# Performance work log

Hardware: AMD Instinct MI355X
Metric: run time of the kernel (lower is better)

The kernel has to match this reference:

```python
import jax, jax.numpy as jnp
import numpy as np

E = 8      # num_experts
K = 2      # num_experts_per_tok
D = 1024   # n_embd
H = 1024   # expert_dim (= 2*n_embd // k)
B, T = 2, 1024


def setup_inputs() -> dict:
    key = jax.random.key(0)
    ks = jax.random.split(key, 6)
    s = 0.02  # weight init scale (keeps relu^2 activations tame)
    return {
        "x": jax.random.normal(ks[0], (B, T, D), dtype=jnp.float32),
        "gate_w": jax.random.normal(ks[1], (E, D), dtype=jnp.float32) * s,
        "lb_bias": jnp.zeros((E,), dtype=jnp.float32),
        "w1": jax.random.normal(ks[2], (E, H, D), dtype=jnp.float32) * s,
        "w2": jax.random.normal(ks[3], (E, D, H), dtype=jnp.float32) * s,
        "cfc": jax.random.normal(ks[4], (H, D), dtype=jnp.float32) * s,
        "cproj": jax.random.normal(ks[5], (D, H), dtype=jnp.float32) * s,
    }


def reference(x, gate_w, lb_bias, w1, w2, cfc, cproj):
    Bx, Tx, Dx = x.shape
    # --- Router: top-k over (logits + load-balance bias), sigmoid gating ---
    logits = jnp.einsum('btd,ed->bte', x, gate_w)               # (B,T,E)
    _, idx = jax.lax.top_k(logits + lb_bias, K)                  # (B,T,K)
    sel_logits = jnp.take_along_axis(logits, idx, axis=-1)       # (B,T,K)
    w = jax.nn.sigmoid(sel_logits)
    w = w / (jnp.sum(w, axis=-1, keepdims=True) + 1e-6)          # (B,T,K)

    # --- Dispatch/combine (dense-equivalent of the per-expert gather loop) ---
    xf = x.reshape(-1, Dx)                                       # (N,D)
    idxf = idx.reshape(-1, K)                                    # (N,K)
    wf = w.reshape(-1, K)                                        # (N,K)
    onehot = jax.nn.one_hot(idxf, E, dtype=wf.dtype)             # (N,K,E)
    we = jnp.einsum('nke,nk->ne', onehot, wf)                    # combined per-expert weight (N,E)

    hidden = jnp.square(jax.nn.relu(jnp.einsum('nd,ehd->neh', xf, w1)))  # (N,E,H)
    expert_out = jnp.einsum('neh,edh->ned', hidden, w2)                  # (N,E,D)
    moe_out = jnp.einsum('ned,ne->nd', expert_out, we).reshape(Bx, Tx, Dx)

    # --- Shared expert (always active): relu(x W1^T)^2 W2^T ---
    sh = jnp.square(jax.nn.relu(jnp.einsum('btd,hd->bth', x, cfc)))
    shared = jnp.einsum('bth,dh->btd', sh, cproj)
    return moe_out + shared
```

## Files before the change

kernel.cpp:

```cpp
#include <hip/hip_runtime.h>
#include <stdint.h>

#define D_DIM 1024
#define H_DIM 1024
#define NE 8
#define NTOK 2048
#define SB 5120
#define TOTAL_ROWS 7168
#define GEMM_BLKS 224
#define CONV2_BLKS 2304
#define M8 (8 * 1024 * 1024)

typedef __bf16 bf16;
typedef bf16 bf16x8 __attribute__((ext_vector_type(8)));
typedef float f32x4 __attribute__((ext_vector_type(4)));

#define GL16(SRC, DST)                                               \
  __builtin_amdgcn_global_load_lds(                                  \
      (const __attribute__((address_space(1))) void*)(SRC),          \
      (__attribute__((address_space(3))) void*)(DST), 16, 0, 0)

#define WS_NTILES     0
#define WS_TILE_E     64
#define WS_TILE_BASE  576
#define WS_EIDX       2048
#define WS_WTOK       18432
#define WS_TOK        34816
#define WS_SLOT       63488
#define WS_XG         131072
#define WS_HID        16777216
#define WS_W1B        33554432
#define WS_W2B        50331648
#define WS_CFCB       67108864
#define WS_CPROJB     69206016

__global__ __launch_bounds__(256) void convrouter(
    const float* __restrict__ x, const float* __restrict__ gw,
    const float* __restrict__ lb, int* __restrict__ eidx,
    float* __restrict__ wtok, bf16* __restrict__ xg,
    const float* __restrict__ w1, const float* __restrict__ cfc,
    bf16* __restrict__ w1b, bf16* __restrict__ cfcb) {
  const int bx = blockIdx.x;
  if (bx >= 512) {
    int i = ((bx - 512) * 256 + threadIdx.x) * 8;
    const float* s;
    bf16* d;
    if (i < M8) { s = w1 + i;        d = w1b + i; }
    else        { s = cfc + (i - M8); d = cfcb + (i - M8); }
    float4 a = *(const float4*)(s);
    float4 b = *(const float4*)(s + 4);
    union { uint4 v; bf16 h[8]; } t;
    t.h[0] = (bf16)a.x; t.h[1] = (bf16)a.y; t.h[2] = (bf16)a.z; t.h[3] = (bf16)a.w;
    t.h[4] = (bf16)b.x; t.h[5] = (bf16)b.y; t.h[6] = (bf16)b.z; t.h[7] = (bf16)b.w;
    *(uint4*)(d) = t.v;
    return;
  }
  const int wave = threadIdx.x >> 6;
  const int lane = threadIdx.x & 63;
  const int n = bx * 4 + wave;

  const float4* xr = (const float4*)(x + (size_t)n * D_DIM);
  float4 xv[4];
#pragma unroll
  for (int q = 0; q < 4; q++) xv[q] = xr[q * 64 + lane];

  float acc[NE];
#pragma unroll
  for (int e = 0; e < NE; e++) acc[e] = 0.f;
#pragma unroll
  for (int e = 0; e < NE; e++) {
    const float4* gr = (const float4*)(gw + e * D_DIM);
#pragma unroll
    for (int q = 0; q < 4; q++) {
      float4 g = gr[q * 64 + lane];
      acc[e] += xv[q].x * g.x + xv[q].y * g.y + xv[q].z * g.z + xv[q].w * g.w;
    }
  }

  bf16* dst = xg + (size_t)n * D_DIM;
#pragma unroll
  for (int q = 0; q < 4; q++) {
    union { ushort4 u; bf16 h[4]; } t;
    t.h[0] = (bf16)xv[q].x; t.h[1] = (bf16)xv[q].y;
    t.h[2] = (bf16)xv[q].z; t.h[3] = (bf16)xv[q].w;
    *(ushort4*)(dst + (q * 64 + lane) * 4) = t.u;
  }

#pragma unroll
  for (int e = 0; e < NE; e++)
#pragma unroll
    for (int off = 32; off > 0; off >>= 1) acc[e] += __shfl_xor(acc[e], off, 64);

  if (lane == 0) {
    float b[NE];
#pragma unroll
    for (int e = 0; e < NE; e++) b[e] = acc[e] + lb[e];
    int i0 = 0; float v0 = b[0];
#pragma unroll
    for (int e = 1; e < NE; e++) if (b[e] > v0) { v0 = b[e]; i0 = e; }
    int i1 = -1; float v1 = -3.4e38f;
#pragma unroll
    for (int e = 0; e < NE; e++) if (e != i0 && b[e] > v1) { v1 = b[e]; i1 = e; }
    float s0 = 1.f / (1.f + expf(-acc[i0]));
    float s1 = 1.f / (1.f + expf(-acc[i1]));
    float s = s0 + s1 + 1e-6f;
    eidx[n * 2] = i0;     wtok[n * 2] = s0 / s;
    eidx[n * 2 + 1] = i1; wtok[n * 2 + 1] = s1 / s;
  }
}

__global__ __launch_bounds__(256) void assign_kernel(
    const int* __restrict__ eidx, int* __restrict__ tE, int* __restrict__ tB,
    int* __restrict__ ntiles, int* __restrict__ tok,
    int* __restrict__ slotIdx) {
  __shared__ int segCnt[64][NE];
  __shared__ int segBase[64][NE];
  const int tid = threadIdx.x;
  const int wave = tid >> 6, lane = tid & 63;
  const unsigned long long below = (lane == 0) ? 0ull : ((~0ull) >> (64 - lane));

  int e16[16], pr16[16];
#pragma unroll
  for (int t = 0; t < 16; t++) {
    const int r = t * 256 + tid;
    const int seg = t * 4 + wave;
    const int e = eidx[r];
    int prior = 0;
#pragma unroll
    for (int ee = 0; ee < NE; ee++) {
      unsigned long long m = __ballot(e == ee);
      if (e == ee) prior = __popcll(m & below);
      if (lane == ee) segCnt[seg][ee] = __popcll(m);
    }
    e16[t] = e; pr16[t] = prior;
  }

  for (int s = tid; s < TOTAL_ROWS; s += 256) {
    tok[s] = (s < SB) ? 0 : (s - SB);
  }
  __syncthreads();

  if (wave == 0) {
    int v[NE], inc[NE];
#pragma unroll
    for (int e = 0; e < NE; e++) { v[e] = segCnt[lane][e]; inc[e] = v[e]; }
#pragma unroll
    for (int off = 1; off < 64; off <<= 1) {
#pragma unroll
      for (int e = 0; e < NE; e++) {
        int u = __shfl_up(inc[e], off);
        if (lane >= off) inc[e] += u;
      }
    }
    int tot[NE];
#pragma unroll
    for (int e = 0; e < NE; e++) tot[e] = __shfl(inc[e], 63);
    int offsL[NE]; int b = 0;
#pragma unroll
    for (int e = 0; e < NE; e++) { offsL[e] = b; b += ((tot[e] + 127) >> 7) << 7; }
#pragma unroll
    for (int e = 0; e < NE; e++) segBase[lane][e] = offsL[e] + (inc[e] - v[e]);
    if (lane == 0) {
      int nt = 0;
      for (int e = 0; e < NE; e++) {
        int t128 = (tot[e] + 127) >> 7;
        for (int t = 0; t < t128; t++) { tE[nt] = e; tB[nt] = offsL[e] + t * 128; nt++; }
      }
      for (int t = 0; t < 16; t++) { tE[nt] = NE; tB[nt] = SB + t * 128; nt++; }
      ntiles[0] = nt;
      ntiles[1] = (nt * 4 + 7) >> 3;
    }
  }
  __syncthreads();

#pragma unroll
  for (int t = 0; t < 16; t++) {
    const int r = t * 256 + tid;
    const int seg = t * 4 + wave;
    const int slot = segBase[seg][e16[t]] + pr16[t];
    tok[slot] = r >> 1;
    slotIdx[r] = slot;
  }
}

template <int MODE>
__global__ __launch_bounds__(512) void moe_gemm(
    const bf16* __restrict__ Ab, const bf16* __restrict__ We,
    const bf16* __restrict__ Ws, const int* __restrict__ tE,
    const int* __restrict__ tB, const int* __restrict__ ntp,
    bf16* __restrict__ Cout, const int* __restrict__ tok,
    const float* __restrict__ cvs1, const float* __restrict__ cvs2,
    bf16* __restrict__ cvd1, bf16* __restrict__ cvd2) {
  if (MODE == 0 && blockIdx.x >= GEMM_BLKS) {
    int i = ((blockIdx.x - GEMM_BLKS) * 512 + threadIdx.x) * 8;
    const float* s;
    bf16* d;
    if (i < M8) { s = cvs1 + i;        d = cvd1 + i; }
    else        { s = cvs2 + (i - M8); d = cvd2 + (i - M8); }
    float4 a = *(const float4*)(s);
    float4 b = *(const float4*)(s + 4);
    union { uint4 v; bf16 h[8]; } t;
    t.h[0] = (bf16)a.x; t.h[1] = (bf16)a.y; t.h[2] = (bf16)a.z; t.h[3] = (bf16)a.w;
    t.h[4] = (bf16)b.x; t.h[5] = (bf16)b.y; t.h[6] = (bf16)b.z; t.h[7] = (bf16)b.w;
    *(uint4*)(d) = t.v;
    return;
  }

  const int per = ntp[1];
  const int g = blockIdx.x & 7, idx = blockIdx.x >> 3;
  if (idx >= per) return;
  const int p = g * per + idx;
  if (p >= ntp[0] * 4) return;
  const int mslot = p >> 2;
  const int n0 = (p & 3) * 256;
  const int e = tE[mslot];
  const int base = tB[mslot];
  const bf16* Bp = (e < NE) ? (We + (size_t)e * (H_DIM * D_DIM)) : Ws;

  __shared__ bf16 As[3 * 4096];
  __shared__ bf16 Bs[3 * 8192];

  const int tid = threadIdx.x;
  const int wave = tid >> 6, lane = tid & 63;

  const int rS = tid >> 2, sS = tid & 3;
  const int cS = sS ^ ((rS >> 1) & 3);
  size_t rowA;
  if (MODE == 0) rowA = tok[base + rS];
  else           rowA = base + rS;
  const bf16* gA  = Ab + rowA * 1024 + cS * 8;
  const bf16* gB1 = Bp + (size_t)(n0 + rS) * 1024 + cS * 8;
  const bf16* gB2 = Bp + (size_t)(n0 + 128 + rS) * 1024 + cS * 8;
  bf16* laBase = As + tid * 8;
  bf16* lbBase = Bs + tid * 8;

  const int wm = (wave >> 2) * 64, wn = (wave & 3) * 64;
  const int fr = lane & 15, chk = lane >> 4;
  int aOff[4], bOff[4];
#pragma unroll
  for (int i = 0; i < 4; i++) {
    const int r = wm + i * 16 + fr;
    aOff[i] = r * 32 + ((chk ^ ((r >> 1) & 3)) * 8);
  }
#pragma unroll
  for (int j = 0; j < 4; j++) {
    const int r = wn + j * 16 + fr;
    bOff[j] = r * 32 + ((chk ^ ((r >> 1) & 3)) * 8);
  }

  const f32x4 zero = {0.f, 0.f, 0.f, 0.f};
  f32x4 acc[4][4];
#pragma unroll
  for (int i = 0; i < 4; i++)
#pragma unroll
    for (int j = 0; j < 4; j++) acc[i][j] = zero;

#pragma unroll
  for (int t = 0; t < 3; ++t) {
    const int ko = t * 32;
    GL16(gA + ko,  laBase + t * 4096);
    GL16(gB1 + ko, lbBase + t * 8192);
    GL16(gB2 + ko, lbBase + t * 8192 + 4096);
  }

#define GEMM_ITER(KT, VMSTR, ISSUE)                                           \
  {                                                                           \
    const int cur = (KT) % 3;                                                 \
    asm volatile("s_waitcnt vmcnt(" VMSTR ")" ::: "memory");                  \
    __builtin_amdgcn_s_barrier();              \
    __builtin_amdgcn_sched_barrier(0);                                        \
    bf16x8 af[4], bv[4];                                                      \
    _Pragma("unroll") for (int i = 0; i < 4; i++)                             \
        af[i] = *(const bf16x8*)&As[cur * 4096 + aOff[i]];                    \
    _Pragma("unroll") for (int j = 0; j < 4; j++)                             \
        bv[j] = *(const bf16x8*)&Bs[cur * 8192 + bOff[j]];                    \
    asm volatile("s_waitcnt lgkmcnt(0)" ::: "memory");                        \
    __builtin_amdgcn_s_barrier();             \
    __builtin_amdgcn_sched_barrier(0);                                        \
    if (ISSUE) {                                                              \
      const int ko = ((KT) + 3) * 32;                                         \
      GL16(gA + ko,  laBase + cur * 4096);                                    \
      GL16(gB1 + ko, lbBase + cur * 8192);                                    \
      GL16(gB2 + ko, lbBase + cur * 8192 + 4096);                             \
    }                                                                         \
    __builtin_amdgcn_s_setprio(1);                                            \
    _Pragma("unroll") for (int i = 0; i < 4; i++)                             \
      _Pragma("unroll") for (int j = 0; j < 4; j++)                           \
          acc[i][j] = __builtin_amdgcn_mfma_f32_16x16x32_bf16(                \
              af[i], bv[j], acc[i][j], 0, 0, 0);                              \
    __builtin_amdgcn_s_setprio(0);                                            \
  }

  for (int kt = 0; kt < 29; ++kt) GEMM_ITER(kt, "6", (kt < 29));
  GEMM_ITER(29, "6", false);
  GEMM_ITER(30, "3", false);
  GEMM_ITER(31, "0", false);
#undef GEMM_ITER

  const int rbase = (lane >> 4) * 4;
#pragma unroll
  for (int i = 0; i < 4; i++) {
#pragma unroll
    for (int j = 0; j < 4; j++) {
      const int col = n0 + wn + j * 16 + fr;
#pragma unroll
      for (int r = 0; r < 4; r++) {
        const int orow = wm + i * 16 + rbase + r;
        float v = acc[i][j][r];
        if (MODE == 0) v = v > 0.f ? v * v : 0.f;
        Cout[(size_t)(base + orow) * 1024 + col] = (bf16)v;
      }
    }
  }
}

__global__ __launch_bounds__(256) void combine_kernel(
    const bf16* __restrict__ eo, const int* __restrict__ slotIdx,
    const float* __restrict__ wtok, float* __restrict__ out) {
  const int t = blockIdx.x;
  const int c = threadIdx.x * 4;
  const int s0 = slotIdx[t * 2], s1 = slotIdx[t * 2 + 1];
  const float w0 = wtok[t * 2], w1 = wtok[t * 2 + 1];
  union U { uint2 v; bf16 h[4]; };
  U a, b, sh;
  a.v  = *(const uint2*)(eo + (size_t)s0 * 1024 + c);
  b.v  = *(const uint2*)(eo + (size_t)s1 * 1024 + c);
  sh.v = *(const uint2*)(eo + (size_t)(SB + t) * 1024 + c);
  float4 o;
  o.x = w0 * (float)a.h[0] + w1 * (float)b.h[0] + (float)sh.h[0];
  o.y = w0 * (float)a.h[1] + w1 * (float)b.h[1] + (float)sh.h[1];
  o.z = w0 * (float)a.h[2] + w1 * (float)b.h[2] + (float)sh.h[2];
  o.w = w0 * (float)a.h[3] + w1 * (float)b.h[3] + (float)sh.h[3];
  *(float4*)(out + (size_t)t * 1024 + c) = o;
}

extern "C" void kernel_launch(void* const* d_in, const int* in_sizes, int n_in,
                              void* d_out, int out_size, void* d_ws,
                              size_t ws_size, hipStream_t stream) {
  const float* x     = (const float*)d_in[0];
  const float* gw    = (const float*)d_in[1];
  const float* lb    = (const float*)d_in[2];
  const float* w1    = (const float*)d_in[3];
  const float* w2    = (const float*)d_in[4];
  const float* cfc   = (const float*)d_in[5];
  const float* cproj = (const float*)d_in[6];
  float* out = (float*)d_out;
  char* ws = (char*)d_ws;

  int*   ntl   = (int*)(ws + WS_NTILES);
  int*   tE    = (int*)(ws + WS_TILE_E);
  int*   tB    = (int*)(ws + WS_TILE_BASE);
  int*   eidx  = (int*)(ws + WS_EIDX);
  float* wtok  = (float*)(ws + WS_WTOK);
  int*   tok   = (int*)(ws + WS_TOK);
  int*   slotI = (int*)(ws + WS_SLOT);
  bf16*  xg    = (bf16*)(ws + WS_XG);
  bf16*  hid   = (bf16*)(ws + WS_HID);
  bf16*  w1b   = (bf16*)(ws + WS_W1B);
  bf16*  w2b   = (bf16*)(ws + WS_W2B);
  bf16*  cfcb  = (bf16*)(ws + WS_CFCB);
  bf16*  cprojb= (bf16*)(ws + WS_CPROJB);

  convrouter<<<5120, 256, 0, stream>>>(x, gw, lb, eidx, wtok, xg,
                                       w1, cfc, w1b, cfcb);
  assign_kernel<<<1, 256, 0, stream>>>(eidx, tE, tB, ntl, tok, slotI);

  moe_gemm<0><<<GEMM_BLKS + CONV2_BLKS, 512, 0, stream>>>(
      xg, w1b, cfcb, tE, tB, ntl, hid, tok, w2, cproj, w2b, cprojb);
  moe_gemm<1><<<GEMM_BLKS, 512, 0, stream>>>(
      hid, w2b, cprojb, tE, tB, ntl, xg, tok, nullptr, nullptr, nullptr, nullptr);
  combine_kernel<<<NTOK, 256, 0, stream>>>(xg, slotI, wtok, out);
}
```

Baseline: 92.00 us.

## Double the GEMM K-tile to 64 and interleave loads with MFMA sub-phases

The grouped-expert GEMM now uses 64-wide K tiles over 16 iterations instead of 32-wide tiles over 32, with an 8-way XOR swizzle and LDS buffers doubled to 144 KB. Each iteration is split into four phases, one per B column fragment, and the global-to-LDS loads for the tile two steps ahead are spread across those phases. The aim is to halve per-K-step barrier and waitcnt overhead and overlap memory traffic with MFMA work. In exchange there are more barriers per iteration, LDS use is much larger (which may cap occupancy at one block per CU), and the vmcnt bookkeeping is fragile.

Result: slower. 95.20 us (+3.5%).

```diff
diff --git a/kernel.cpp b/kernel.cpp
--- a/kernel.cpp
+++ b/kernel.cpp
@@ -14,6 +14,8 @@
 typedef __bf16 bf16;
 typedef bf16 bf16x8 __attribute__((ext_vector_type(8)));
 typedef float f32x4 __attribute__((ext_vector_type(4)));
+
+#define MFMA16(A, B, C) __builtin_amdgcn_mfma_f32_16x16x32_bf16((A), (B), (C), 0, 0, 0)
 
 #define GL16(SRC, DST)                                               \
   __builtin_amdgcn_global_load_lds(                                  \
@@ -217,20 +219,26 @@
   const int base = tB[mslot];
   const bf16* Bp = (e < NE) ? (We + (size_t)e * (H_DIM * D_DIM)) : Ws;
 
-  __shared__ bf16 As[3 * 4096];
-  __shared__ bf16 Bs[3 * 8192];
+  __shared__ bf16 As[3 * 8192];
+  __shared__ bf16 Bs[3 * 16384];
 
   const int tid = threadIdx.x;
   const int wave = tid >> 6, lane = tid & 63;
 
-  const int rS = tid >> 2, sS = tid & 3;
-  const int cS = sS ^ ((rS >> 1) & 3);
-  size_t rowA;
-  if (MODE == 0) rowA = tok[base + rS];
-  else           rowA = base + rS;
-  const bf16* gA  = Ab + rowA * 1024 + cS * 8;
-  const bf16* gB1 = Bp + (size_t)(n0 + rS) * 1024 + cS * 8;
-  const bf16* gB2 = Bp + (size_t)(n0 + 128 + rS) * 1024 + cS * 8;
+  const int rS = tid >> 3, cP = tid & 7;
+  const int colS = (cP ^ (rS & 7)) * 8;
+  const bf16* gA[2];
+  const bf16* gB[4];
+#pragma unroll
+  for (int q = 0; q < 2; q++) {
+    size_t rowA;
+    if (MODE == 0) rowA = tok[base + 64 * q + rS];
+    else           rowA = base + 64 * q + rS;
+    gA[q] = Ab + rowA * 1024 + colS;
+  }
+#pragma unroll
+  for (int q = 0; q < 4; q++)
+    gB[q] = Bp + (size_t)(n0 + 64 * q + rS) * 1024 + colS;
   bf16* laBase = As + tid * 8;
   bf16* lbBase = Bs + tid * 8;
 
@@ -240,12 +248,12 @@
 #pragma unroll
   for (int i = 0; i < 4; i++) {
     const int r = wm + i * 16 + fr;
-    aOff[i] = r * 32 + ((chk ^ ((r >> 1) & 3)) * 8);
+    aOff[i] = r * 64 + ((chk ^ (r & 7)) * 8);
   }
 #pragma unroll
   for (int j = 0; j < 4; j++) {
     const int r = wn + j * 16 + fr;
-    bOff[j] = r * 32 + ((chk ^ ((r >> 1) & 3)) * 8);
+    bOff[j] = r * 64 + ((chk ^ (r & 7)) * 8);
   }
 
   const f32x4 zero = {0.f, 0.f, 0.f, 0.f};
@@ -256,46 +264,79 @@
     for (int j = 0; j < 4; j++) acc[i][j] = zero;
 
 #pragma unroll
-  for (int t = 0; t < 3; ++t) {
-    const int ko = t * 32;
-    GL16(gA + ko,  laBase + t * 4096);
-    GL16(gB1 + ko, lbBase + t * 8192);
-    GL16(gB2 + ko, lbBase + t * 8192 + 4096);
-  }
-
-#define GEMM_ITER(KT, VMSTR, ISSUE)                                           \
-  {                                                                           \
-    const int cur = (KT) % 3;                                                 \
-    asm volatile("s_waitcnt vmcnt(" VMSTR ")" ::: "memory");                  \
-    __builtin_amdgcn_s_barrier();              \
-    __builtin_amdgcn_sched_barrier(0);                                        \
-    bf16x8 af[4], bv[4];                                                      \
-    _Pragma("unroll") for (int i = 0; i < 4; i++)                             \
-        af[i] = *(const bf16x8*)&As[cur * 4096 + aOff[i]];                    \
-    _Pragma("unroll") for (int j = 0; j < 4; j++)                             \
-        bv[j] = *(const bf16x8*)&Bs[cur * 8192 + bOff[j]];                    \
-    asm volatile("s_waitcnt lgkmcnt(0)" ::: "memory");                        \
-    __builtin_amdgcn_s_barrier();             \
-    __builtin_amdgcn_sched_barrier(0);                                        \
-    if (ISSUE) {                                                              \
-      const int ko = ((KT) + 3) * 32;                                         \
-      GL16(gA + ko,  laBase + cur * 4096);                                    \
-      GL16(gB1 + ko, lbBase + cur * 8192);                                    \
-      GL16(gB2 + ko, lbBase + cur * 8192 + 4096);                             \
-    }                                                                         \
-    __builtin_amdgcn_s_setprio(1);                                            \
-    _Pragma("unroll") for (int i = 0; i < 4; i++)                             \
-      _Pragma("unroll") for (int j = 0; j < 4; j++)                           \
-          acc[i][j] = __builtin_amdgcn_mfma_f32_16x16x32_bf16(                \
-              af[i], bv[j], acc[i][j], 0, 0, 0);                              \
-    __builtin_amdgcn_s_setprio(0);                                            \
-  }
-
-  for (int kt = 0; kt < 29; ++kt) GEMM_ITER(kt, "6", (kt < 29));
-  GEMM_ITER(29, "6", false);
-  GEMM_ITER(30, "3", false);
-  GEMM_ITER(31, "0", false);
-#undef GEMM_ITER
+  for (int t = 0; t < 2; ++t) {
+    const int ko = t * 64;
+    GL16(gA[0] + ko, laBase + t * 8192);
+    GL16(gA[1] + ko, laBase + t * 8192 + 4096);
+#pragma unroll
+    for (int q = 0; q < 4; q++)
+      GL16(gB[q] + ko, lbBase + t * 16384 + q * 4096);
+  }
+  asm volatile("s_waitcnt vmcnt(6)" ::: "memory");
+  __builtin_amdgcn_s_barrier();
+  __builtin_amdgcn_sched_barrier(0);
+
+  for (int kt = 0; kt < 16; ++kt) {
+    const int cur = kt % 3;
+    const int nxt = (kt + 2) % 3;
+    const bool issue = (kt < 14);
+    const int ko = (kt + 2) * 64;
+    const bf16* Ac = As + cur * 8192;
+    const bf16* Bc = Bs + cur * 16384;
+
+    bf16x8 af[4][2], b0, b1;
+#pragma unroll
+    for (int i = 0; i < 4; i++) {
+      af[i][0] = *(const bf16x8*)&Ac[aOff[i]];
+      af[i][1] = *(const bf16x8*)&Ac[aOff[i] ^ 32];
+    }
+    b0 = *(const bf16x8*)&Bc[bOff[0]];
+    b1 = *(const bf16x8*)&Bc[bOff[0] ^ 32];
+    if (issue) {
+      GL16(gA[0] + ko, laBase + nxt * 8192);
+      GL16(gA[1] + ko, laBase + nxt * 8192 + 4096);
+    }
+    __builtin_amdgcn_s_barrier();
+    asm volatile("s_waitcnt lgkmcnt(0)" ::: "memory");
+    __builtin_amdgcn_sched_barrier(0);
+    __builtin_amdgcn_s_setprio(1);
+#pragma unroll
+    for (int i = 0; i < 4; i++) {
+      acc[i][0] = MFMA16(af[i][0], b0, acc[i][0]);
+      acc[i][0] = MFMA16(af[i][1], b1, acc[i][0]);
+    }
+    __builtin_amdgcn_s_setprio(0);
+    __builtin_amdgcn_s_barrier();
+
+#pragma unroll
+    for (int j = 1; j < 4; j++) {
+      b0 = *(const bf16x8*)&Bc[bOff[j]];
+      b1 = *(const bf16x8*)&Bc[bOff[j] ^ 32];
+      if (issue) {
+        if (j == 1) {
+          GL16(gB[0] + ko, lbBase + nxt * 16384);
+          GL16(gB[1] + ko, lbBase + nxt * 16384 + 4096);
+        }
+        if (j == 2) GL16(gB[2] + ko, lbBase + nxt * 16384 + 8192);
+        if (j == 3) GL16(gB[3] + ko, lbBase + nxt * 16384 + 12288);
+      }
+      if (j == 3) {
+        if (kt < 14)       asm volatile("s_waitcnt vmcnt(6)" ::: "memory");
+        else if (kt == 14) asm volatile("s_waitcnt vmcnt(0)" ::: "memory");
+      }
+      __builtin_amdgcn_s_barrier();
+      asm volatile("s_waitcnt lgkmcnt(0)" ::: "memory");
+      __builtin_amdgcn_sched_barrier(0);
+      __builtin_amdgcn_s_setprio(1);
+#pragma unroll
+      for (int i = 0; i < 4; i++) {
+        acc[i][j] = MFMA16(af[i][0], b0, acc[i][j]);
+        acc[i][j] = MFMA16(af[i][1], b1, acc[i][j]);
+      }
+      __builtin_amdgcn_s_setprio(0);
+      __builtin_amdgcn_s_barrier();
+    }
+  }
 
   const int rbase = (lane >> 4) * 4;
 #pragma unroll
```
